# Kernel optimization log

Measured on AMD Instinct MI355X. Metric: run time of the kernel, lower is better.

## Reference

```python
import jax, jax.numpy as jnp
import numpy as np

LEAKY_SLOPE = 0.2

def setup_inputs() -> dict:
    key = jax.random.key(0)
    k1, k2, k3, k4, k5 = jax.random.split(key, 5)
    N, F_IN, H, D = 8192, 256, 4, 64
    x = jax.random.normal(k1, (N, F_IN), dtype=jnp.float32)
    adj = jax.random.randint(k2, (N, N), 0, 2, dtype=jnp.int32)
    W = jax.random.normal(k3, (F_IN, H * D), dtype=jnp.float32) * 0.05
    a_l = jax.random.normal(k4, (H, D), dtype=jnp.float32) * 0.05
    a_r = jax.random.normal(k5, (H, D), dtype=jnp.float32) * 0.05
    return {"x": x, "adj": adj, "W": W, "a_l": a_l, "a_r": a_r}

def reference(x, adj, W, a_l, a_r):
    N = x.shape[0]
    H, D = a_l.shape
    # projected node features: (N, H, D)
    h = (x @ W).reshape(N, H, D)
    score_l = jnp.einsum('nhd,hd->nh', h, a_l)  # (N, H)
    score_r = jnp.einsum('nhd,hd->nh', h, a_r)  # (N, H)
    # logits[i, j, h] = score_l[i, h] + score_r[j, h]
    logits = score_l[:, None, :] + score_r[None, :, :]
    logits = jax.nn.leaky_relu(logits, negative_slope=LEAKY_SLOPE)
    # mask: keep edge (i,j) if adj[i,j] + eye[i,j] != 0
    keep = (adj + jnp.eye(N, dtype=adj.dtype)) != 0  # (N, N)
    logits = jnp.where(keep[:, :, None], logits, -jnp.inf)
    # softmax over neighbors j (axis=1), matching torch softmax(dim=1)
    attn = jax.nn.softmax(logits, axis=1)  # (N, N, H)
    out = jnp.einsum('ijh,jhf->ihf', attn, h)  # (N, H, D)
    return out.reshape(N, H * D)  # concat=True
```

## Files before the change

kernel.cpp:

```cpp
#include <hip/hip_runtime.h>
#include <hip/hip_bf16.h>
#include <hip/hip_fp16.h>

#define N 8192
#define FIN 256
#define HD 256
#define LEAKY 0.2f

typedef short sh8 __attribute__((ext_vector_type(8)));
typedef _Float16 h8 __attribute__((ext_vector_type(8)));
typedef _Float16 h2 __attribute__((ext_vector_type(2)));
typedef float f32x4 __attribute__((ext_vector_type(4)));
typedef int   i32x4 __attribute__((ext_vector_type(4)));

__device__ __forceinline__ int pack2bf(float a, float b){
  __hip_bfloat162 t = __float22bfloat162_rn(make_float2(a, b));
  union { __hip_bfloat162 h; int i; } u;
  u.h = t;
  return u.i;
}

__device__ __forceinline__ h2 u2h2(unsigned u){ union{unsigned u; h2 h;} c; c.u=u; return c.h; }
__device__ __forceinline__ unsigned h22u(h2 h){ union{unsigned u; h2 h;} c; c.h=h; return c.u; }

__global__ void k_wt(const float* __restrict__ W, __hip_bfloat16* __restrict__ Wt){
  __shared__ float t[16][17];
  int tx = threadIdx.x, ty = threadIdx.y;
  int bx = blockIdx.x*16, by = blockIdx.y*16;
  t[ty][tx] = W[(by+ty)*HD + (bx+tx)];
  __syncthreads();
  Wt[(bx+ty)*FIN + (by+tx)] = __float2bfloat16(t[tx][ty]);
}

__global__ __launch_bounds__(256, 2) void k_h(
    const float* __restrict__ x, const __hip_bfloat16* __restrict__ Wt,
    const float* __restrict__ a_l, const float* __restrict__ a_r,
    _Float16* __restrict__ ht, float* __restrict__ El, float* __restrict__ El2,
    _Float16* __restrict__ Erh, _Float16* __restrict__ Er2h)
{
  const int lane = threadIdx.x & 63;
  const int w = threadIdx.x >> 6;
  const int r0 = lane & 15, q = lane >> 4;
  const int c0 = w*64;
  const int n0 = blockIdx.x*32;

  f32x4 acc[4][2];
  #pragma unroll
  for (int m = 0; m < 4; ++m)
    #pragma unroll
    for (int nt = 0; nt < 2; ++nt)
      acc[m][nt] = (f32x4){0.f, 0.f, 0.f, 0.f};

  for (int kb = 0; kb < 8; ++kb){
    const int k = kb*32 + q*8;
    sh8 af[4];
    #pragma unroll
    for (int m = 0; m < 4; ++m)
      af[m] = *(const sh8*)(Wt + (c0 + m*16 + r0)*FIN + k);
    #pragma unroll
    for (int nt = 0; nt < 2; ++nt){
      const float* xp = x + (n0 + nt*16 + r0)*FIN + k;
      f32x4 xl = *(const f32x4*)xp;
      f32x4 xh = *(const f32x4*)(xp + 4);
      union { sh8 s; int i[4]; } bx;
      bx.i[0] = pack2bf(xl[0], xl[1]);
      bx.i[1] = pack2bf(xl[2], xl[3]);
      bx.i[2] = pack2bf(xh[0], xh[1]);
      bx.i[3] = pack2bf(xh[2], xh[3]);
      #pragma unroll
      for (int m = 0; m < 4; ++m)
        acc[m][nt] = __builtin_amdgcn_mfma_f32_16x16x32_bf16(af[m], bx.s, acc[m][nt], 0, 0, 0);
    }
  }

  float pl[2] = {0.f, 0.f}, pr[2] = {0.f, 0.f};
  #pragma unroll
  for (int m = 0; m < 4; ++m){
    #pragma unroll
    for (int reg = 0; reg < 4; ++reg){
      const int c = c0 + m*16 + q*4 + reg;
      const float alv = a_l[c], arv = a_r[c];
      #pragma unroll
      for (int nt = 0; nt < 2; ++nt){
        float v = acc[m][nt][reg];
        ht[(size_t)c*N + (n0 + nt*16 + r0)] = (_Float16)v;
        pl[nt] += v*alv;
        pr[nt] += v*arv;
      }
    }
  }
  #pragma unroll
  for (int nt = 0; nt < 2; ++nt){
    pl[nt] += __shfl_xor(pl[nt], 16); pl[nt] += __shfl_xor(pl[nt], 32);
    pr[nt] += __shfl_xor(pr[nt], 16); pr[nt] += __shfl_xor(pr[nt], 32);
  }
  if (lane < 16){
    #pragma unroll
    for (int nt = 0; nt < 2; ++nt){
      const int n = n0 + nt*16 + r0;
      const float l = pl[nt], r = pr[nt];
      El  [w*N + n] = __expf(l);
      El2 [w*N + n] = __expf(LEAKY*l);
      Erh [w*N + n] = (_Float16)__expf(r);
      Er2h[w*N + n] = (_Float16)__expf(LEAKY*r);
    }
  }
}

__global__ __launch_bounds__(256, 4) void k_attn(
    const int* __restrict__ adj, const _Float16* __restrict__ ht,
    const float* __restrict__ El, const float* __restrict__ El2,
    const _Float16* __restrict__ Erh, const _Float16* __restrict__ Er2h,
    float* __restrict__ part, float* __restrict__ zpart)
{
  __shared__ __align__(16) char smem[32768];
  const int b = blockIdx.x;
  const int h = b >> 8, jq = (b >> 6) & 3, i128 = b & 63;
  const int tid = threadIdx.x;
  const int lane = tid & 63;
  const int w = tid >> 6;
  const int r0 = lane & 15, q = lane >> 4;
  const int ib = i128*128 + w*32;
  const int jbase = jq * 2048;

  const _Float16* gp = ht + (size_t)(h*64 + w*16 + (lane >> 2))*N
                          + jbase + (((lane & 3) ^ ((lane >> 3) & 3))*8);
  char* lb = smem + w*1024;
  const char* frp = smem + r0*64 + ((q ^ ((r0 >> 1) & 3)) << 4);

  const float* el_ = El  + h*N + ib + r0;
  const float* el2_= El2 + h*N + ib + r0;
  h2 elh[2], el2h[2];
  #pragma unroll
  for (int m = 0; m < 2; ++m){
    _Float16 a = (_Float16)el_[m*16];
    _Float16 c = (_Float16)el2_[m*16];
    elh[m]  = (h2){a, a};
    el2h[m] = (h2){c, c};
  }
  const _Float16* erq  = Erh  + h*N + jbase + q*8;
  const _Float16* er2q = Er2h + h*N + jbase + q*8;

  const int* ap0 = adj + (size_t)(ib + r0)*N + jbase + q*8;
  const int* ap1 = ap0 + 16*N;

  int td[2], sd[2], pd[2];
  unsigned eyem[2];
  bool db[2];
  #pragma unroll
  for (int m = 0; m < 2; ++m){
    const int am = ib + m*16;
    db[m] = ((am >> 11) == jq);
    td[m] = (am >> 7) & 15;
    sd[m] = (am >> 5) & 3;
    const int dr = (am & 31) + r0;
    pd[m] = (dr & 7) >> 1;
    eyem[m] = ((dr >> 3) == q) ? ((dr & 1) ? 0x10000u : 1u) : 0u;
  }

  union { h8 s; int i[4]; } onef;
  {
    int v = (r0 == 0) ? 0x3C003C00 : 0;
    onef.i[0]=v; onef.i[1]=v; onef.i[2]=v; onef.i[3]=v;
  }

  f32x4 acc[2][4];
  f32x4 accz[2];
  #pragma unroll
  for (int m = 0; m < 2; ++m){
    accz[m] = (f32x4){0.f,0.f,0.f,0.f};
    #pragma unroll
    for (int d = 0; d < 4; ++d)
      acc[m][d] = (f32x4){0.f,0.f,0.f,0.f};
  }

#define STAGE(bufoff, t) do { \
    const _Float16* _g = gp + (t)*128; \
    _Pragma("unroll") \
    for (int _s = 0; _s < 4; ++_s) \
      __builtin_amdgcn_global_load_lds( \
        (const __attribute__((address_space(1))) void*)(_g + _s*32), \
        (__attribute__((address_space(3))) void*)(lb + (bufoff) + _s*4096), 16, 0, 0); \
  } while(0)

#define LD_ADJ(dst, off) do { \
    dst[0][0] = *(const i32x4*)(ap0 + (off)); \
    dst[0][1] = *(const i32x4*)(ap0 + (off) + 4); \
    dst[1][0] = *(const i32x4*)(ap1 + (off)); \
    dst[1][1] = *(const i32x4*)(ap1 + (off) + 4); \
  } while(0)

  i32x4 ac[2][2], an[2][2];
  LD_ADJ(ac, 0);
  STAGE(0, 0);
  __syncthreads();

  for (int t = 0; t < 16; ++t){
    const int bo = (t & 1) ? 16384 : 0;
    const int bn = bo ^ 16384;
    const int tn = (t + 1) & 15;
    STAGE(bn, tn);

    #pragma unroll
    for (int ss = 0; ss < 4; ++ss){
      const int noff = (ss < 3) ? (t*128 + (ss+1)*32) : (tn*128);
      LD_ADJ(an, noff);

      i32x4 er4  = *(const i32x4*)(erq  + t*128 + ss*32);
      i32x4 er24 = *(const i32x4*)(er2q + t*128 + ss*32);

      h8 hf[4];
      #pragma unroll
      for (int d = 0; d < 4; ++d)
        hf[d] = *(const h8*)(frp + bo + ss*4096 + d*1024);

      #pragma unroll
      for (int m = 0; m < 2; ++m){
        const bool dg = db[m] && (t == td[m]) && (ss == sd[m]);
        unsigned fu[4];
        #pragma unroll
        for (int p = 0; p < 4; ++p){
          const int a0 = ac[m][p >> 1][(p & 1)*2];
          const int a1 = ac[m][p >> 1][(p & 1)*2 + 1];
          unsigned t32 = (unsigned)a0 | ((unsigned)a1 << 16);
          if (dg) t32 |= (p == pd[m]) ? eyem[m] : 0u;
          const unsigned msk = t32 * 0xFFFFu;
          h2 w2 = __builtin_elementwise_max(elh[m]  * u2h2((unsigned)er4[p]),
                                            el2h[m] * u2h2((unsigned)er24[p]));
          fu[p] = h22u(w2) & msk;
        }
        union { h8 s; unsigned u[4]; } fa;
        fa.u[0]=fu[0]; fa.u[1]=fu[1]; fa.u[2]=fu[2]; fa.u[3]=fu[3];
        #pragma unroll
        for (int d = 0; d < 4; ++d)
          acc[m][d] = __builtin_amdgcn_mfma_f32_16x16x32_f16(fa.s, hf[d], acc[m][d], 0, 0, 0);
        accz[m] = __builtin_amdgcn_mfma_f32_16x16x32_f16(fa.s, onef.s, accz[m], 0, 0, 0);
      }

      #pragma unroll
      for (int m = 0; m < 2; ++m){
        ac[m][0] = an[m][0]; ac[m][1] = an[m][1];
      }
    }

    __syncthreads();
  }

  if (r0 == 0){
    #pragma unroll
    for (int m = 0; m < 2; ++m)
      #pragma unroll
      for (int reg = 0; reg < 4; ++reg)
        zpart[(jq*4 + h)*N + ib + m*16 + q*4 + reg] = accz[m][reg];
  }

  float* pp = part + (size_t)jq*N*HD + h*64 + r0;
  #pragma unroll
  for (int m = 0; m < 2; ++m)
    #pragma unroll
    for (int d = 0; d < 4; ++d)
      #pragma unroll
      for (int reg = 0; reg < 4; ++reg)
        pp[(size_t)(ib + m*16 + q*4 + reg)*HD + d*16] = acc[m][d][reg];
#undef STAGE
#undef LD_ADJ
}

__global__ void k_out(const float* __restrict__ part, const float* __restrict__ zpart,
                      float* __restrict__ out)
{
  const int t4 = (blockIdx.x*256 + threadIdx.x) * 4;
  const int i = t4 >> 8;
  const int h = (t4 & 255) >> 6;
  f32x4 a = *(const f32x4*)(part + t4);
  f32x4 bq = *(const f32x4*)(part + (size_t)N*HD + t4);
  f32x4 c = *(const f32x4*)(part + 2*(size_t)N*HD + t4);
  f32x4 d = *(const f32x4*)(part + 3*(size_t)N*HD + t4);
  float zz = zpart[h*N + i] + zpart[(4 + h)*N + i] + zpart[(8 + h)*N + i] + zpart[(12 + h)*N + i];
  f32x4 s = (a + bq + c + d) / zz;
  *(f32x4*)(out + t4) = s;
}

extern "C" void kernel_launch(void* const* d_in, const int* in_sizes, int n_in,
                              void* d_out, int out_size, void* d_ws, size_t ws_size,
                              hipStream_t stream) {
  const float* x   = (const float*)d_in[0];
  const int*   adj = (const int*)d_in[1];
  const float* W   = (const float*)d_in[2];
  const float* a_l = (const float*)d_in[3];
  const float* a_r = (const float*)d_in[4];
  float* out = (float*)d_out;

  char* ws = (char*)d_ws;
  __hip_bfloat16* Wt = (__hip_bfloat16*)ws;
  _Float16* ht   = (_Float16*)(ws + 131072);
  float*    El   = (float*)   (ws + 4325376);
  float*    El2  = (float*)   (ws + 4456448);
  _Float16* Erh  = (_Float16*)(ws + 4587520);
  _Float16* Er2h = (_Float16*)(ws + 4653056);
  float*    part = (float*)   (ws + 4718592);
  float*    zpart= (float*)   (ws + 38273024);

  k_wt  <<<dim3(16,16), dim3(16,16), 0, stream>>>(W, Wt);
  k_h   <<<256, 256, 0, stream>>>(x, Wt, a_l, a_r, ht, El, El2, Erh, Er2h);
  k_attn<<<1024, 256, 0, stream>>>(adj, ht, El, El2, Erh, Er2h, part, zpart);
  k_out <<<N*HD/1024, 256, 0, stream>>>(part, zpart, out);
}
```

Baseline: 477.6 us.

## Pre-pack adjacency into bitmask and stage Er vectors in LDS

Adds a pre-pass kernel that compresses the int32 adjacency matrix, with the self-loop folded in, into a bitmask laid out to match the MFMA fragment order. The attention kernel then reads the bitmask instead of the full int adjacency, which it previously read once for each of the 4 heads, so adjacency traffic in that kernel drops sharply. The Er and Er2 vectors are loaded into LDS once per block, and the projection kernel is split into smaller 16-row blocks to get more parallelism. The cost is an extra full pass over the 256MB adjacency matrix plus one more launch.

```diff
diff --git a/kernel.cpp b/kernel.cpp
--- a/kernel.cpp
+++ b/kernel.cpp
@@ -30,6 +30,30 @@
   t[ty][tx] = W[(by+ty)*HD + (bx+tx)];
   __syncthreads();
   Wt[(bx+ty)*FIN + (by+tx)] = __float2bfloat16(t[tx][ty]);
+}
+
+__global__ __launch_bounds__(256) void k_pack(const int* __restrict__ adj,
+                                              unsigned* __restrict__ bits){
+  const int t = blockIdx.x*256 + threadIdx.x;
+  const int i = t >> 8;
+  const int c = t & 255;
+  const int* p = adj + (size_t)i*N + c*32;
+  unsigned w = 0;
+  #pragma unroll
+  for (int v = 0; v < 8; ++v){
+    i32x4 a = *(const i32x4*)(p + v*4);
+    #pragma unroll
+    for (int e = 0; e < 4; ++e){
+      const int k = v*4 + e;
+      const unsigned pos = (unsigned)((k >> 1) + ((k & 1) << 4));
+      w |= ((unsigned)a[e] & 1u) << pos;
+    }
+  }
+  if ((i >> 5) == c){
+    const int k = i & 31;
+    w |= 1u << ((k >> 1) + ((k & 1) << 4));
+  }
+  bits[t] = w;
 }
 
 __global__ __launch_bounds__(256, 2) void k_h(
@@ -42,14 +66,11 @@
   const int w = threadIdx.x >> 6;
   const int r0 = lane & 15, q = lane >> 4;
   const int c0 = w*64;
-  const int n0 = blockIdx.x*32;
-
-  f32x4 acc[4][2];
-  #pragma unroll
-  for (int m = 0; m < 4; ++m)
-    #pragma unroll
-    for (int nt = 0; nt < 2; ++nt)
-      acc[m][nt] = (f32x4){0.f, 0.f, 0.f, 0.f};
+  const int n0 = blockIdx.x*16;
+
+  f32x4 acc[4];
+  #pragma unroll
+  for (int m = 0; m < 4; ++m) acc[m] = (f32x4){0.f, 0.f, 0.f, 0.f};
 
   for (int kb = 0; kb < 8; ++kb){
     const int k = kb*32 + q*8;
@@ -57,63 +78,49 @@
     #pragma unroll
     for (int m = 0; m < 4; ++m)
       af[m] = *(const sh8*)(Wt + (c0 + m*16 + r0)*FIN + k);
-    #pragma unroll
-    for (int nt = 0; nt < 2; ++nt){
-      const float* xp = x + (n0 + nt*16 + r0)*FIN + k;
-      f32x4 xl = *(const f32x4*)xp;
-      f32x4 xh = *(const f32x4*)(xp + 4);
-      union { sh8 s; int i[4]; } bx;
-      bx.i[0] = pack2bf(xl[0], xl[1]);
-      bx.i[1] = pack2bf(xl[2], xl[3]);
-      bx.i[2] = pack2bf(xh[0], xh[1]);
-      bx.i[3] = pack2bf(xh[2], xh[3]);
-      #pragma unroll
-      for (int m = 0; m < 4; ++m)
-        acc[m][nt] = __builtin_amdgcn_mfma_f32_16x16x32_bf16(af[m], bx.s, acc[m][nt], 0, 0, 0);
-    }
-  }
-
-  float pl[2] = {0.f, 0.f}, pr[2] = {0.f, 0.f};
+    const float* xp = x + (n0 + r0)*FIN + k;
+    f32x4 xl = *(const f32x4*)xp;
+    f32x4 xh = *(const f32x4*)(xp + 4);
+    union { sh8 s; int i[4]; } bx;
+    bx.i[0] = pack2bf(xl[0], xl[1]);
+    bx.i[1] = pack2bf(xl[2], xl[3]);
+    bx.i[2] = pack2bf(xh[0], xh[1]);
+    bx.i[3] = pack2bf(xh[2], xh[3]);
+    #pragma unroll
+    for (int m = 0; m < 4; ++m)
+      acc[m] = __builtin_amdgcn_mfma_f32_16x16x32_bf16(af[m], bx.s, acc[m], 0, 0, 0);
+  }
+
+  float pl = 0.f, pr = 0.f;
   #pragma unroll
   for (int m = 0; m < 4; ++m){
     #pragma unroll
     for (int reg = 0; reg < 4; ++reg){
       const int c = c0 + m*16 + q*4 + reg;
-      const float alv = a_l[c], arv = a_r[c];
-      #pragma unroll
-      for (int nt = 0; nt < 2; ++nt){
-        float v = acc[m][nt][reg];
-        ht[(size_t)c*N + (n0 + nt*16 + r0)] = (_Float16)v;
-        pl[nt] += v*alv;
-        pr[nt] += v*arv;
-      }
+      const float v = acc[m][reg];
+      ht[(size_t)c*N + (n0 + r0)] = (_Float16)v;
+      pl += v*a_l[c];
+      pr += v*a_r[c];
     }
   }
-  #pragma unroll
-  for (int nt = 0; nt < 2; ++nt){
-    pl[nt] += __shfl_xor(pl[nt], 16); pl[nt] += __shfl_xor(pl[nt], 32);
-    pr[nt] += __shfl_xor(pr[nt], 16); pr[nt] += __shfl_xor(pr[nt], 32);
-  }
+  pl += __shfl_xor(pl, 16); pl += __shfl_xor(pl, 32);
+  pr += __shfl_xor(pr, 16); pr += __shfl_xor(pr, 32);
   if (lane < 16){
-    #pragma unroll
-    for (int nt = 0; nt < 2; ++nt){
-      const int n = n0 + nt*16 + r0;
-      const float l = pl[nt], r = pr[nt];
-      El  [w*N + n] = __expf(l);
-      El2 [w*N + n] = __expf(LEAKY*l);
-      Erh [w*N + n] = (_Float16)__expf(r);
-      Er2h[w*N + n] = (_Float16)__expf(LEAKY*r);
-    }
+    const int n = n0 + r0;
+    El  [w*N + n] = __expf(pl);
+    El2 [w*N + n] = __expf(LEAKY*pl);
+    Erh [w*N + n] = (_Float16)__expf(pr);
+    Er2h[w*N + n] = (_Float16)__expf(LEAKY*pr);
   }
 }
 
 __global__ __launch_bounds__(256, 4) void k_attn(
-    const int* __restrict__ adj, const _Float16* __restrict__ ht,
+    const unsigned* __restrict__ bits, const _Float16* __restrict__ ht,
     const float* __restrict__ El, const float* __restrict__ El2,
     const _Float16* __restrict__ Erh, const _Float16* __restrict__ Er2h,
     float* __restrict__ part, float* __restrict__ zpart)
 {
-  __shared__ __align__(16) char smem[32768];
+  __shared__ __align__(16) char smem[40960];
   const int b = blockIdx.x;
   const int h = b >> 8, jq = (b >> 6) & 3, i128 = b & 63;
   const int tid = threadIdx.x;
@@ -128,6 +135,19 @@
   char* lb = smem + w*1024;
   const char* frp = smem + r0*64 + ((q ^ ((r0 >> 1) & 3)) << 4);
 
+  {
+    const _Float16* s1 = Erh  + h*N + jbase + w*512 + lane*8;
+    const _Float16* s2 = Er2h + h*N + jbase + w*512 + lane*8;
+    __builtin_amdgcn_global_load_lds(
+      (const __attribute__((address_space(1))) void*)s1,
+      (__attribute__((address_space(3))) void*)(smem + 32768 + w*1024), 16, 0, 0);
+    __builtin_amdgcn_global_load_lds(
+      (const __attribute__((address_space(1))) void*)s2,
+      (__attribute__((address_space(3))) void*)(smem + 36864 + w*1024), 16, 0, 0);
+  }
+  const char* erp1 = smem + 32768 + q*16;
+  const char* erp2 = smem + 36864 + q*16;
+
   const float* el_ = El  + h*N + ib + r0;
   const float* el2_= El2 + h*N + ib + r0;
   h2 elh[2], el2h[2];
@@ -138,25 +158,10 @@
     elh[m]  = (h2){a, a};
     el2h[m] = (h2){c, c};
   }
-  const _Float16* erq  = Erh  + h*N + jbase + q*8;
-  const _Float16* er2q = Er2h + h*N + jbase + q*8;
-
-  const int* ap0 = adj + (size_t)(ib + r0)*N + jbase + q*8;
-  const int* ap1 = ap0 + 16*N;
-
-  int td[2], sd[2], pd[2];
-  unsigned eyem[2];
-  bool db[2];
-  #pragma unroll
-  for (int m = 0; m < 2; ++m){
-    const int am = ib + m*16;
-    db[m] = ((am >> 11) == jq);
-    td[m] = (am >> 7) & 15;
-    sd[m] = (am >> 5) & 3;
-    const int dr = (am & 31) + r0;
-    pd[m] = (dr & 7) >> 1;
-    eyem[m] = ((dr >> 3) == q) ? ((dr & 1) ? 0x10000u : 1u) : 0u;
-  }
+
+  const unsigned* bp0 = bits + (size_t)(ib + r0)*(N/32) + jq*64;
+  const unsigned* bp1 = bp0 + 16*(N/32);
+  const int qs = q*4;
 
   union { h8 s; int i[4]; } onef;
   {
@@ -183,15 +188,9 @@
         (__attribute__((address_space(3))) void*)(lb + (bufoff) + _s*4096), 16, 0, 0); \
   } while(0)
 
-#define LD_ADJ(dst, off) do { \
-    dst[0][0] = *(const i32x4*)(ap0 + (off)); \
-    dst[0][1] = *(const i32x4*)(ap0 + (off) + 4); \
-    dst[1][0] = *(const i32x4*)(ap1 + (off)); \
-    dst[1][1] = *(const i32x4*)(ap1 + (off) + 4); \
-  } while(0)
-
-  i32x4 ac[2][2], an[2][2];
-  LD_ADJ(ac, 0);
+  i32x4 bcur[2], bnxt[2];
+  bcur[0] = *(const i32x4*)(bp0);
+  bcur[1] = *(const i32x4*)(bp1);
   STAGE(0, 0);
   __syncthreads();
 
@@ -200,14 +199,13 @@
     const int bn = bo ^ 16384;
     const int tn = (t + 1) & 15;
     STAGE(bn, tn);
+    bnxt[0] = *(const i32x4*)(bp0 + tn*4);
+    bnxt[1] = *(const i32x4*)(bp1 + tn*4);
 
     #pragma unroll
     for (int ss = 0; ss < 4; ++ss){
-      const int noff = (ss < 3) ? (t*128 + (ss+1)*32) : (tn*128);
-      LD_ADJ(an, noff);
-
-      i32x4 er4  = *(const i32x4*)(erq  + t*128 + ss*32);
-      i32x4 er24 = *(const i32x4*)(er2q + t*128 + ss*32);
+      i32x4 er4  = *(const i32x4*)(erp1 + t*256 + ss*64);
+      i32x4 er24 = *(const i32x4*)(erp2 + t*256 + ss*64);
 
       h8 hf[4];
       #pragma unroll
@@ -216,14 +214,11 @@
 
       #pragma unroll
       for (int m = 0; m < 2; ++m){
-        const bool dg = db[m] && (t == td[m]) && (ss == sd[m]);
+        const unsigned wq = ((unsigned)bcur[m][ss]) >> qs;
         unsigned fu[4];
         #pragma unroll
         for (int p = 0; p < 4; ++p){
-          const int a0 = ac[m][p >> 1][(p & 1)*2];
-          const int a1 = ac[m][p >> 1][(p & 1)*2 + 1];
-          unsigned t32 = (unsigned)a0 | ((unsigned)a1 << 16);
-          if (dg) t32 |= (p == pd[m]) ? eyem[m] : 0u;
+          const unsigned t32 = (wq >> p) & 0x10001u;
           const unsigned msk = t32 * 0xFFFFu;
           h2 w2 = __builtin_elementwise_max(elh[m]  * u2h2((unsigned)er4[p]),
                                             el2h[m] * u2h2((unsigned)er24[p]));
@@ -236,13 +231,9 @@
           acc[m][d] = __builtin_amdgcn_mfma_f32_16x16x32_f16(fa.s, hf[d], acc[m][d], 0, 0, 0);
         accz[m] = __builtin_amdgcn_mfma_f32_16x16x32_f16(fa.s, onef.s, accz[m], 0, 0, 0);
       }
-
-      #pragma unroll
-      for (int m = 0; m < 2; ++m){
-        ac[m][0] = an[m][0]; ac[m][1] = an[m][1];
-      }
     }
 
+    bcur[0] = bnxt[0]; bcur[1] = bnxt[1];
     __syncthreads();
   }
 
@@ -263,7 +254,6 @@
       for (int reg = 0; reg < 4; ++reg)
         pp[(size_t)(ib + m*16 + q*4 + reg)*HD + d*16] = acc[m][d][reg];
 #undef STAGE
-#undef LD_ADJ
 }
 
 __global__ void k_out(const float* __restrict__ part, const float* __restrict__ zpart,
@@ -300,9 +290,11 @@
   _Float16* Er2h = (_Float16*)(ws + 4653056);
   float*    part = (float*)   (ws + 4718592);
   float*    zpart= (float*)   (ws + 38273024);
+  unsigned* bits = (unsigned*)(ws + 38797312);
 
   k_wt  <<<dim3(16,16), dim3(16,16), 0, stream>>>(W, Wt);
-  k_h   <<<256, 256, 0, stream>>>(x, Wt, a_l, a_r, ht, El, El2, Erh, Er2h);
-  k_attn<<<1024, 256, 0, stream>>>(adj, ht, El, El2, Erh, Er2h, part, zpart);
+  k_pack<<<N*N/32/256, 256, 0, stream>>>(adj, bits);
+  k_h   <<<512, 256, 0, stream>>>(x, Wt, a_l, a_r, ht, El, El2, Erh, Er2h);
+  k_attn<<<1024, 256, 0, stream>>>(bits, ht, El, El2, Erh, Er2h, part, zpart);
   k_out <<<N*HD/1024, 256, 0, stream>>>(part, zpart, out);
 }
```

New measurement: 441.7 us. 1.08x faster.
